# Performance work log

Measured on AMD Instinct MI355X. Metric: run time of the kernel, lower is better.

The kernel has to match this reference:

```python
import jax, jax.numpy as jnp
import numpy as np

N_NODES, N_EDGES, N_GRAPHS = 20000, 320000, 64
D_IN, D_H, D_FC, OUT_DIMS = 1280, 512, 1024, 5000
BN_EPS = 1e-5


def setup_inputs() -> dict:
    key = jax.random.key(0)
    ks = jax.random.split(key, 12)
    sc = lambda k, s: (jax.random.normal(k, s, jnp.float32) * 0.02)
    return {
        "x": jax.random.normal(ks[0], (N_NODES, D_IN), jnp.float32),
        "edge_index": jax.random.randint(ks[1], (2, N_EDGES), 0, N_NODES, dtype=jnp.int64),
        "batch": jnp.sort(jax.random.randint(ks[2], (N_NODES,), 0, N_GRAPHS, dtype=jnp.int64)),
        "Wg1": sc(ks[3], (D_IN, D_H)),
        "bg1": jnp.zeros((D_H,), jnp.float32),
        "Wg2": sc(ks[4], (D_H, D_H)),
        "bg2": jnp.zeros((D_H,), jnp.float32),
        "W1": sc(ks[5], (D_H, D_FC)),
        "b1": jnp.zeros((D_FC,), jnp.float32),
        "W2": sc(ks[6], (D_FC, OUT_DIMS)),
        "b2": jnp.zeros((OUT_DIMS,), jnp.float32),
        "gamma": jnp.ones((OUT_DIMS,), jnp.float32),
        "beta": jnp.zeros((OUT_DIMS,), jnp.float32),
    }


def _gcn_conv(h_in, W, b, src, dst):
    # PyG GCNConv: linear transform, symmetric deg^{-1/2} normalization with self-loops.
    h = h_in @ W  # [N, D]
    ones = jnp.ones((src.shape[0],), h.dtype)
    deg = jax.ops.segment_sum(ones, dst, num_segments=N_NODES) + 1.0  # self-loop
    dinv = jax.lax.rsqrt(deg)  # [N]
    coef = dinv[src] * dinv[dst]  # [E]
    agg = jax.ops.segment_sum(h[src] * coef[:, None], dst, num_segments=N_NODES)
    agg = agg + h * (dinv * dinv)[:, None]  # self-loop contribution
    return agg + b


def reference(x, edge_index, batch, Wg1, bg1, Wg2, bg2, W1, b1, W2, b2, gamma, beta):
    src, dst = edge_index[0], edge_index[1]
    h = jax.nn.relu(_gcn_conv(x, Wg1, bg1, src, dst))
    h = jax.nn.relu(_gcn_conv(h, Wg2, bg2, src, dst))
    # global max pool over each graph in the batch
    g = jax.ops.segment_max(h, batch, num_segments=N_GRAPHS)  # [G, 512]
    # fc head (eval mode: dropout = identity, BatchNorm1d uses running stats mean=0, var=1)
    h1 = jax.nn.relu(g @ W1 + b1)
    logits = h1 @ W2 + b2
    bn = logits * (gamma / jnp.sqrt(1.0 + BN_EPS)) + beta
    return jax.nn.sigmoid(bn)
```

## Files before the change

kernel.cpp:

```cpp
#include <hip/hip_runtime.h>
#include <math.h>

#define N_NODES 20000
#define N_EDGES 320000
#define N_GRAPHS 64
#define D_IN 1280
#define D_H 512
#define D_FC 1024
#define OUT_DIMS 5000
#define BKT_CAP 64
#define PSPLIT 8

typedef unsigned short ushort_t;
typedef short bf16x8 __attribute__((ext_vector_type(8)));
typedef float f32x4 __attribute__((ext_vector_type(4)));

__device__ __forceinline__ ushort_t f2b(float x) {
    unsigned u = __float_as_uint(x);
    unsigned r = (u + 0x7FFFu + ((u >> 16) & 1u)) >> 16;
    return (ushort_t)r;
}

#define WAITVM(n) asm volatile("s_waitcnt vmcnt(" #n ")" ::: "memory")
#define WAITLG() asm volatile("s_waitcnt lgkmcnt(0)" ::: "memory")
#define SCHED0() __builtin_amdgcn_sched_barrier(0)

#define GLL16(gp, lp)                                                                  \
    __builtin_amdgcn_global_load_lds((const __attribute__((address_space(1))) void*)(gp), \
                                     (__attribute__((address_space(3))) void*)(lp), 16, 0, 0)

__global__ __launch_bounds__(64) void mfma_gemm_1w(const ushort_t* __restrict__ A,
                                                   const ushort_t* __restrict__ BT,
                                                   ushort_t* __restrict__ C,
                                                   int M, int N, int K) {
    __shared__ ushort_t lds[8192];
    const int lane = threadIdx.x;
    const int lo = lane & 15, quad = lane >> 4;

    const int bid = blockIdx.x;
    const int v = (bid & 7) * 313 + (bid >> 3);
    const int rowBase = (v >> 3) * 64;
    const int colBase = (v & 7) * 64;

    const int q = (lane & 3) ^ ((lane >> 3) & 3);
    const int rb = lane >> 2;
    const ushort_t* pa[4];
    const ushort_t* pb[4];
#pragma unroll
    for (int i = 0; i < 4; ++i) {
        int ar = rowBase + rb + 16 * i;
        if (ar >= M) ar = M - 1;
        pa[i] = A + (size_t)ar * K + q * 8;
        pb[i] = BT + (size_t)(colBase + rb + 16 * i) * K + q * 8;
    }

#define ISSUE_TILE(p)                                      \
    {                                                      \
        GLL16(pa[0], lds + (p) * 2048 + 0 * 512);          \
        GLL16(pa[1], lds + (p) * 2048 + 1 * 512);          \
        GLL16(pa[2], lds + (p) * 2048 + 2 * 512);          \
        GLL16(pa[3], lds + (p) * 2048 + 3 * 512);          \
        GLL16(pb[0], lds + 4096 + (p) * 2048 + 0 * 512);   \
        GLL16(pb[1], lds + 4096 + (p) * 2048 + 1 * 512);   \
        GLL16(pb[2], lds + 4096 + (p) * 2048 + 2 * 512);   \
        GLL16(pb[3], lds + 4096 + (p) * 2048 + 3 * 512);   \
        pa[0] += 32; pa[1] += 32; pa[2] += 32; pa[3] += 32; \
        pb[0] += 32; pb[1] += 32; pb[2] += 32; pb[3] += 32; \
    }

    const int qs = (quad ^ ((lo >> 1) & 3)) * 8;
    int offA[4], offB[4];
#pragma unroll
    for (int i = 0; i < 4; ++i) offA[i] = (i * 16 + lo) * 32 + qs;
#pragma unroll
    for (int j = 0; j < 4; ++j) offB[j] = (j * 16 + lo) * 32 + qs;

    f32x4 acc[4][4] = {};
    const int NK = K >> 5;

    ISSUE_TILE(0);
    ISSUE_TILE(1);

    for (int k = 0; k < NK; ++k) {
        if (k + 1 < NK) { WAITVM(8); } else { WAITVM(0); }
        const ushort_t* Ab = lds + (k & 1) * 2048;
        const ushort_t* Bb = lds + 4096 + (k & 1) * 2048;
        bf16x8 af[4], bfr[4];
#pragma unroll
        for (int i = 0; i < 4; ++i) af[i] = *(const bf16x8*)&Ab[offA[i]];
#pragma unroll
        for (int j = 0; j < 4; ++j) bfr[j] = *(const bf16x8*)&Bb[offB[j]];
        WAITLG();
        if (k + 2 < NK) { ISSUE_TILE(k & 1); }
        SCHED0();
#pragma unroll
        for (int i = 0; i < 4; ++i)
#pragma unroll
            for (int j = 0; j < 4; ++j)
                acc[i][j] = __builtin_amdgcn_mfma_f32_16x16x32_bf16(af[i], bfr[j], acc[i][j], 0, 0, 0);
    }
#undef ISSUE_TILE

#pragma unroll
    for (int i = 0; i < 4; ++i) {
        int row0 = rowBase + i * 16 + quad * 4;
#pragma unroll
        for (int j = 0; j < 4; ++j) {
            int col = colBase + j * 16 + lo;
            if (col >= N) continue;
#pragma unroll
            for (int r = 0; r < 4; ++r) {
                int row = row0 + r;
                if (row < M) C[(size_t)row * N + col] = f2b(acc[i][j][r]);
            }
        }
    }
}

#define PREP_ZB 5
#define PREP_T1 640
#define PREP_T2 256
#define PREP_XB 12500
#define PREP_NBLK (PREP_ZB + PREP_T1 + PREP_T2 + PREP_XB + 1)

__global__ __launch_bounds__(256) void prep_all(const float* __restrict__ W1src, ushort_t* __restrict__ w1t,
                                                const float* __restrict__ W2src, ushort_t* __restrict__ w2t,
                                                const float* __restrict__ x, ushort_t* __restrict__ xb,
                                                int* __restrict__ zbase,
                                                const int* __restrict__ batch, int* __restrict__ gstart) {
    __shared__ float tile[32][33];
    int b = blockIdx.x;
    const int t = threadIdx.x;

    if (b < PREP_ZB) {
        int i = b * 256 + t;
        if (i < 1250) {
            int4* p = (int4*)zbase + (size_t)i * 4;
            int4 z = {0, 0, 0, 0};
            p[0] = z; p[1] = z; p[2] = z; p[3] = z;
        }
        return;
    }
    b -= PREP_ZB;

    if (b < PREP_T1 + PREP_T2) {
        const float* W;
        ushort_t* WT;
        int K, N, tb;
        if (b < PREP_T1) { W = W1src; WT = w1t; K = D_IN; N = D_H; tb = b; }
        else             { W = W2src; WT = w2t; K = D_H;  N = D_H; tb = b - PREP_T1; }
        const int ntn = N >> 5;
        const int kt = tb / ntn, nt = tb - kt * ntn;
        const int tx = t & 31, ty = t >> 5;
#pragma unroll
        for (int it = 0; it < 4; ++it) {
            int k = kt * 32 + ty + it * 8;
            tile[ty + it * 8][tx] = W[(size_t)k * N + nt * 32 + tx];
        }
        __syncthreads();
#pragma unroll
        for (int it = 0; it < 4; ++it) {
            int n = nt * 32 + ty + it * 8;
            WT[(size_t)n * K + kt * 32 + tx] = f2b(tile[tx][ty + it * 8]);
        }
        return;
    }
    b -= PREP_T1 + PREP_T2;

    if (b < PREP_XB) {
        int i = b * 256 + t;
        const float4* p = (const float4*)(x + (size_t)i * 8);
        float4 v0 = p[0], v1 = p[1];
        ushort_t w[8] = {f2b(v0.x), f2b(v0.y), f2b(v0.z), f2b(v0.w),
                         f2b(v1.x), f2b(v1.y), f2b(v1.z), f2b(v1.w)};
        *(uint4*)(xb + (size_t)i * 8) = *(uint4*)w;
        return;
    }

    if (t <= N_GRAPHS) {
        int lo = 0, hi = N_NODES;
        while (lo < hi) {
            int mid = (lo + hi) >> 1;
            if (batch[mid] < t) lo = mid + 1; else hi = mid;
        }
        gstart[t] = lo;
    }
}

__global__ void fill_bucket(const int* __restrict__ src, const int* __restrict__ dst,
                            int* __restrict__ cursor, int* __restrict__ col) {
    int e = blockIdx.x * blockDim.x + threadIdx.x;
    if (e < N_EDGES) {
        int d = dst[e];
        int p = atomicAdd(cursor + d, 1);
        if (p < BKT_CAP) col[(d << 6) + p] = src[e];
    }
}

__global__ void compute_dinv(const int* __restrict__ deg, float* __restrict__ dinv) {
    int v = blockIdx.x * blockDim.x + threadIdx.x;
    if (v < N_NODES) dinv[v] = rsqrtf((float)deg[v] + 1.0f);
}

__global__ __launch_bounds__(256) void gemm_splitk(const float* __restrict__ A,
                                                   const float* __restrict__ B,
                                                   float* __restrict__ P,
                                                   int M, int N, int K, int KC) {
    __shared__ float As[16][64];
    __shared__ float Bs[16][64];
    const int t = threadIdx.x;
    const int tx = t & 15, ty = t >> 4;
    const int rowBase = blockIdx.y * 64;
    const int colBase = blockIdx.x * 64;
    const int kbeg = blockIdx.z * KC;
    const int kend = kbeg + KC;
    float acc[4][4] = {};
    for (int k0 = kbeg; k0 < kend; k0 += 16) {
#pragma unroll
        for (int i = 0; i < 4; ++i) {
            int idx = t + i * 256;
            int row = idx >> 4, kk = idx & 15;
            int gr = rowBase + row;
            As[kk][row] = (gr < M) ? A[(size_t)gr * K + k0 + kk] : 0.f;
        }
#pragma unroll
        for (int i = 0; i < 4; ++i) {
            int idx = t + i * 256;
            int kk = idx >> 6, col = idx & 63;
            int gc = colBase + col;
            Bs[kk][col] = (gc < N) ? B[(size_t)(k0 + kk) * N + gc] : 0.f;
        }
        __syncthreads();
#pragma unroll
        for (int kk = 0; kk < 16; ++kk) {
            float a[4], bb[4];
#pragma unroll
            for (int i = 0; i < 4; ++i) a[i] = As[kk][ty * 4 + i];
#pragma unroll
            for (int j = 0; j < 4; ++j) bb[j] = Bs[kk][tx * 4 + j];
#pragma unroll
            for (int i = 0; i < 4; ++i)
#pragma unroll
                for (int j = 0; j < 4; ++j) acc[i][j] = fmaf(a[i], bb[j], acc[i][j]);
        }
        __syncthreads();
    }
    float* Pz = P + (size_t)blockIdx.z * M * N;
#pragma unroll
    for (int i = 0; i < 4; ++i) {
        int gr = rowBase + ty * 4 + i;
        if (gr >= M) continue;
#pragma unroll
        for (int j = 0; j < 4; ++j) {
            int gc = colBase + tx * 4 + j;
            if (gc < N) Pz[(size_t)gr * N + gc] = acc[i][j];
        }
    }
}

__global__ void reduce_bias_relu(const float* __restrict__ P, const float* __restrict__ b,
                                 float* __restrict__ out, int total, int N, int S) {
    int i = blockIdx.x * blockDim.x + threadIdx.x;
    if (i >= total) return;
    float s = 0.f;
    for (int z = 0; z < S; ++z) s += P[(size_t)z * total + i];
    out[i] = fmaxf(s + b[i % N], 0.f);
}

__global__ void reduce_bn_sigmoid(const float* __restrict__ P, const float* __restrict__ b2,
                                  const float* __restrict__ gamma, const float* __restrict__ beta,
                                  float* __restrict__ out, int S) {
    int i = blockIdx.x * blockDim.x + threadIdx.x;
    if (i >= N_GRAPHS * OUT_DIMS) return;
    int c = i % OUT_DIMS;
    float s = 0.f;
    for (int z = 0; z < S; ++z) s += P[(size_t)z * N_GRAPHS * OUT_DIMS + i];
    const float sc = 0.9999950000374997f;
    float zz = (s + b2[c]) * (gamma[c] * sc) + beta[c];
    out[i] = 1.f / (1.f + expf(-zz));
}

__device__ __forceinline__ void bf8_fma(uint4 v, float c, float* acc) {
    unsigned a[4] = {v.x, v.y, v.z, v.w};
#pragma unroll
    for (int i = 0; i < 4; ++i) {
        float lo = __uint_as_float(a[i] << 16);
        float hi = __uint_as_float(a[i] & 0xFFFF0000u);
        acc[2 * i]     = fmaf(lo, c, acc[2 * i]);
        acc[2 * i + 1] = fmaf(hi, c, acc[2 * i + 1]);
    }
}

__device__ __forceinline__ void agg_node_bf16(const ushort_t* __restrict__ H,
                                              const int* __restrict__ deg,
                                              const int* __restrict__ col,
                                              const float* __restrict__ dinv,
                                              const float* __restrict__ bias,
                                              int v, int f, float* r) {
    const int beg = v << 6;
    int d = deg[v]; if (d > BKT_CAP) d = BKT_CAP;
    const int end = beg + d;
    const float dv = dinv[v];
    float acc[8] = {};
    int j = beg;
    for (; j + 7 < end; j += 8) {
        int s[8];
#pragma unroll
        for (int u = 0; u < 8; ++u) s[u] = col[j + u];
        float c[8];
#pragma unroll
        for (int u = 0; u < 8; ++u) c[u] = dinv[s[u]] * dv;
        uint4 h[8];
#pragma unroll
        for (int u = 0; u < 8; ++u) h[u] = *(const uint4*)(H + (size_t)s[u] * D_H + f);
#pragma unroll
        for (int u = 0; u < 8; ++u) bf8_fma(h[u], c[u], acc);
    }
    for (; j + 3 < end; j += 4) {
        int s0 = col[j], s1 = col[j + 1], s2 = col[j + 2], s3 = col[j + 3];
        float c0 = dinv[s0] * dv, c1 = dinv[s1] * dv;
        float c2 = dinv[s2] * dv, c3 = dinv[s3] * dv;
        uint4 h0 = *(const uint4*)(H + (size_t)s0 * D_H + f);
        uint4 h1 = *(const uint4*)(H + (size_t)s1 * D_H + f);
        uint4 h2 = *(const uint4*)(H + (size_t)s2 * D_H + f);
        uint4 h3 = *(const uint4*)(H + (size_t)s3 * D_H + f);
        bf8_fma(h0, c0, acc);
        bf8_fma(h1, c1, acc);
        bf8_fma(h2, c2, acc);
        bf8_fma(h3, c3, acc);
    }
    for (; j < end; ++j) {
        int s0 = col[j];
        float c0 = dinv[s0] * dv;
        uint4 h0 = *(const uint4*)(H + (size_t)s0 * D_H + f);
        bf8_fma(h0, c0, acc);
    }
    uint4 hv = *(const uint4*)(H + (size_t)v * D_H + f);
    bf8_fma(hv, dv * dv, acc);
    float4 b0 = *(const float4*)(bias + f);
    float4 b1 = *(const float4*)(bias + f + 4);
    r[0] = fmaxf(acc[0] + b0.x, 0.f);
    r[1] = fmaxf(acc[1] + b0.y, 0.f);
    r[2] = fmaxf(acc[2] + b0.z, 0.f);
    r[3] = fmaxf(acc[3] + b0.w, 0.f);
    r[4] = fmaxf(acc[4] + b1.x, 0.f);
    r[5] = fmaxf(acc[5] + b1.y, 0.f);
    r[6] = fmaxf(acc[6] + b1.z, 0.f);
    r[7] = fmaxf(acc[7] + b1.w, 0.f);
}

__global__ __launch_bounds__(256) void gather_agg_relu_bf16(const ushort_t* __restrict__ H,
                                                            const int* __restrict__ deg,
                                                            const int* __restrict__ col,
                                                            const float* __restrict__ dinv,
                                                            const float* __restrict__ bias,
                                                            ushort_t* __restrict__ out) {
    const int v = blockIdx.x * 4 + (threadIdx.x >> 6);
    const int f = (threadIdx.x & 63) * 8;
    float r[8];
    agg_node_bf16(H, deg, col, dinv, bias, v, f, r);
    ushort_t o[8];
#pragma unroll
    for (int i = 0; i < 8; ++i) o[i] = f2b(r[i]);
    *(uint4*)(out + (size_t)v * D_H + f) = *(uint4*)o;
}

__global__ __launch_bounds__(256) void pool_max_partial(const ushort_t* __restrict__ h2,
                                                        const int* __restrict__ gstart,
                                                        float* __restrict__ pbuf) {
    const int g = blockIdx.x;
    const int s = blockIdx.y;
    const int f = threadIdx.x * 2;
    const int beg = gstart[g], end = gstart[g + 1];
    const int len = end - beg;
    const int chunk = (len + PSPLIT - 1) / PSPLIT;
    int lo = beg + s * chunk;
    int hi = lo + chunk; if (hi > end) hi = end;
    float m0 = -INFINITY, m1 = -INFINITY;
    int v = lo;
    for (; v + 3 < hi; v += 4) {
        unsigned u0 = *(const unsigned*)(h2 + (size_t)(v + 0) * D_H + f);
        unsigned u1 = *(const unsigned*)(h2 + (size_t)(v + 1) * D_H + f);
        unsigned u2 = *(const unsigned*)(h2 + (size_t)(v + 2) * D_H + f);
        unsigned u3 = *(const unsigned*)(h2 + (size_t)(v + 3) * D_H + f);
        m0 = fmaxf(m0, fmaxf(fmaxf(__uint_as_float(u0 << 16), __uint_as_float(u1 << 16)),
                             fmaxf(__uint_as_float(u2 << 16), __uint_as_float(u3 << 16))));
        m1 = fmaxf(m1, fmaxf(fmaxf(__uint_as_float(u0 & 0xFFFF0000u), __uint_as_float(u1 & 0xFFFF0000u)),
                             fmaxf(__uint_as_float(u2 & 0xFFFF0000u), __uint_as_float(u3 & 0xFFFF0000u))));
    }
    for (; v < hi; ++v) {
        unsigned u = *(const unsigned*)(h2 + (size_t)v * D_H + f);
        m0 = fmaxf(m0, __uint_as_float(u << 16));
        m1 = fmaxf(m1, __uint_as_float(u & 0xFFFF0000u));
    }
    float* p = pbuf + ((size_t)s * N_GRAPHS + g) * D_H + f;
    p[0] = m0;
    p[1] = m1;
}

__global__ void pool_max_final(const float* __restrict__ pbuf, float* __restrict__ gbuf) {
    int i = blockIdx.x * blockDim.x + threadIdx.x;
    if (i >= N_GRAPHS * D_H) return;
    float m = -INFINITY;
#pragma unroll
    for (int s = 0; s < PSPLIT; ++s) m = fmaxf(m, pbuf[(size_t)s * N_GRAPHS * D_H + i]);
    gbuf[i] = m;
}

extern "C" void kernel_launch(void* const* d_in, const int* in_sizes, int n_in,
                              void* d_out, int out_size, void* d_ws, size_t ws_size,
                              hipStream_t stream) {
    const float* x     = (const float*)d_in[0];
    const int*   ei    = (const int*)d_in[1];
    const int*   batch = (const int*)d_in[2];
    const float* Wg1   = (const float*)d_in[3];
    const float* bg1   = (const float*)d_in[4];
    const float* Wg2   = (const float*)d_in[5];
    const float* bg2   = (const float*)d_in[6];
    const float* W1    = (const float*)d_in[7];
    const float* b1    = (const float*)d_in[8];
    const float* W2    = (const float*)d_in[9];
    const float* b2    = (const float*)d_in[10];
    const float* gamma = (const float*)d_in[11];
    const float* beta  = (const float*)d_in[12];
    const int* src = ei;
    const int* dst = ei + N_EDGES;
    float* out = (float*)d_out;

    const int S1 = 8;
    const int S2 = 8;

    ushort_t* hpre   = (ushort_t*)d_ws;
    ushort_t* h1b    = hpre + (size_t)N_NODES * D_H;
    ushort_t* w1t    = h1b + (size_t)N_NODES * D_H;
    ushort_t* w2t    = w1t + (size_t)D_H * D_IN;
    ushort_t* xb     = w2t + (size_t)D_H * D_H;
    float*    dinv   = (float*)(xb + (size_t)N_NODES * D_IN);
    float*    gbuf   = dinv + N_NODES;
    float*    pbuf   = gbuf + N_GRAPHS * D_H;
    float*    fc1o   = pbuf + (size_t)PSPLIT * N_GRAPHS * D_H;
    float*    part1  = fc1o + N_GRAPHS * D_FC;
    float*    part2  = part1 + (size_t)S1 * N_GRAPHS * D_FC;
    int*      cursor = (int*)(part2 + (size_t)S2 * N_GRAPHS * OUT_DIMS);
    int*      colbkt = cursor + N_NODES;
    int*      gstart = colbkt + (size_t)N_NODES * BKT_CAP;

    prep_all<<<PREP_NBLK, 256, 0, stream>>>(Wg1, w1t, Wg2, w2t, x, xb, cursor, batch, gstart);

    fill_bucket<<<(N_EDGES + 255) / 256, 256, 0, stream>>>(src, dst, cursor, colbkt);
    compute_dinv<<<(N_NODES + 255) / 256, 256, 0, stream>>>(cursor, dinv);

    const int gconv = 2504;

    mfma_gemm_1w<<<gconv, 64, 0, stream>>>(xb, w1t, hpre, N_NODES, D_H, D_IN);
    gather_agg_relu_bf16<<<N_NODES / 4, 256, 0, stream>>>(hpre, cursor, colbkt, dinv, bg1, h1b);

    mfma_gemm_1w<<<gconv, 64, 0, stream>>>(h1b, w2t, hpre, N_NODES, D_H, D_H);
    gather_agg_relu_bf16<<<N_NODES / 4, 256, 0, stream>>>(hpre, cursor, colbkt, dinv, bg2, h1b);
    pool_max_partial<<<dim3(N_GRAPHS, PSPLIT), 256, 0, stream>>>(h1b, gstart, pbuf);
    pool_max_final<<<(N_GRAPHS * D_H + 255) / 256, 256, 0, stream>>>(pbuf, gbuf);

    dim3 gfc1((D_FC + 63) / 64, 1, S1);
    gemm_splitk<<<gfc1, 256, 0, stream>>>(gbuf, W1, part1, N_GRAPHS, D_FC, D_H, D_H / S1);
    reduce_bias_relu<<<(N_GRAPHS * D_FC + 255) / 256, 256, 0, stream>>>(
        part1, b1, fc1o, N_GRAPHS * D_FC, D_FC, S1);

    dim3 gfc2((OUT_DIMS + 63) / 64, 1, S2);
    gemm_splitk<<<gfc2, 256, 0, stream>>>(fc1o, W2, part2, N_GRAPHS, OUT_DIMS, D_FC, D_FC / S2);
    reduce_bn_sigmoid<<<(N_GRAPHS * OUT_DIMS + 255) / 256, 256, 0, stream>>>(
        part2, b2, gamma, beta, out, S2);
}
```

Measured before the change: 444.1 us.

## Fuse fp32-to-bf16 conversion of x into first GEMM and load operands directly

Drops the separate pass that converts x to bf16 and writes an xb buffer. The first GCN GEMM now reads fp32 x directly and converts it in registers with v_cvt_pk_bf16_f32. Both GEMMs stop staging tiles through LDS with global_load_lds and instead load MFMA fragments straight from global memory into registers, double-buffered. This saves the 51 MB x round trip and the LDS staging, but fp32 A loads double the bytes each block reads for A, and the per-lane direct loads are less coalesced with no LDS reuse.

Result: slower. 546.7 us (+23.1%).

```diff
diff --git a/kernel.cpp b/kernel.cpp
--- a/kernel.cpp
+++ b/kernel.cpp
@@ -21,85 +21,69 @@
     return (ushort_t)r;
 }
 
-#define WAITVM(n) asm volatile("s_waitcnt vmcnt(" #n ")" ::: "memory")
-#define WAITLG() asm volatile("s_waitcnt lgkmcnt(0)" ::: "memory")
-#define SCHED0() __builtin_amdgcn_sched_barrier(0)
-
-#define GLL16(gp, lp)                                                                  \
-    __builtin_amdgcn_global_load_lds((const __attribute__((address_space(1))) void*)(gp), \
-                                     (__attribute__((address_space(3))) void*)(lp), 16, 0, 0)
-
-__global__ __launch_bounds__(64) void mfma_gemm_1w(const ushort_t* __restrict__ A,
-                                                   const ushort_t* __restrict__ BT,
-                                                   ushort_t* __restrict__ C,
-                                                   int M, int N, int K) {
-    __shared__ ushort_t lds[8192];
+__device__ __forceinline__ unsigned cvt_pk(float lo, float hi) {
+    unsigned r;
+    asm("v_cvt_pk_bf16_f32 %0, %1, %2" : "=v"(r) : "v"(lo), "v"(hi));
+    return r;
+}
+
+__global__ __launch_bounds__(64) void gemm_dir_bf16(const ushort_t* __restrict__ A,
+                                                    const ushort_t* __restrict__ BT,
+                                                    ushort_t* __restrict__ C,
+                                                    int M, int N, int K) {
     const int lane = threadIdx.x;
     const int lo = lane & 15, quad = lane >> 4;
-
     const int bid = blockIdx.x;
     const int v = (bid & 7) * 313 + (bid >> 3);
     const int rowBase = (v >> 3) * 64;
     const int colBase = (v & 7) * 64;
 
-    const int q = (lane & 3) ^ ((lane >> 3) & 3);
-    const int rb = lane >> 2;
     const ushort_t* pa[4];
     const ushort_t* pb[4];
 #pragma unroll
     for (int i = 0; i < 4; ++i) {
-        int ar = rowBase + rb + 16 * i;
-        if (ar >= M) ar = M - 1;
-        pa[i] = A + (size_t)ar * K + q * 8;
-        pb[i] = BT + (size_t)(colBase + rb + 16 * i) * K + q * 8;
-    }
-
-#define ISSUE_TILE(p)                                      \
-    {                                                      \
-        GLL16(pa[0], lds + (p) * 2048 + 0 * 512);          \
-        GLL16(pa[1], lds + (p) * 2048 + 1 * 512);          \
-        GLL16(pa[2], lds + (p) * 2048 + 2 * 512);          \
-        GLL16(pa[3], lds + (p) * 2048 + 3 * 512);          \
-        GLL16(pb[0], lds + 4096 + (p) * 2048 + 0 * 512);   \
-        GLL16(pb[1], lds + 4096 + (p) * 2048 + 1 * 512);   \
-        GLL16(pb[2], lds + 4096 + (p) * 2048 + 2 * 512);   \
-        GLL16(pb[3], lds + 4096 + (p) * 2048 + 3 * 512);   \
-        pa[0] += 32; pa[1] += 32; pa[2] += 32; pa[3] += 32; \
-        pb[0] += 32; pb[1] += 32; pb[2] += 32; pb[3] += 32; \
-    }
-
-    const int qs = (quad ^ ((lo >> 1) & 3)) * 8;
-    int offA[4], offB[4];
-#pragma unroll
-    for (int i = 0; i < 4; ++i) offA[i] = (i * 16 + lo) * 32 + qs;
-#pragma unroll
-    for (int j = 0; j < 4; ++j) offB[j] = (j * 16 + lo) * 32 + qs;
+        int r = rowBase + i * 16 + lo;
+        if (r >= M) r = M - 1;
+        pa[i] = A + (size_t)r * K + quad * 8;
+        pb[i] = BT + (size_t)(colBase + i * 16 + lo) * K + quad * 8;
+    }
 
     f32x4 acc[4][4] = {};
     const int NK = K >> 5;
 
-    ISSUE_TILE(0);
-    ISSUE_TILE(1);
-
-    for (int k = 0; k < NK; ++k) {
-        if (k + 1 < NK) { WAITVM(8); } else { WAITVM(0); }
-        const ushort_t* Ab = lds + (k & 1) * 2048;
-        const ushort_t* Bb = lds + 4096 + (k & 1) * 2048;
-        bf16x8 af[4], bfr[4];
-#pragma unroll
-        for (int i = 0; i < 4; ++i) af[i] = *(const bf16x8*)&Ab[offA[i]];
-#pragma unroll
-        for (int j = 0; j < 4; ++j) bfr[j] = *(const bf16x8*)&Bb[offB[j]];
-        WAITLG();
-        if (k + 2 < NK) { ISSUE_TILE(k & 1); }
-        SCHED0();
+    bf16x8 a0[4], b0[4], a1[4], b1[4];
+#pragma unroll
+    for (int i = 0; i < 4; ++i) {
+        a0[i] = *(const bf16x8*)(pa[i]);
+        b0[i] = *(const bf16x8*)(pb[i]);
+    }
+
+    for (int kk = 0; kk < NK; kk += 2) {
+#pragma unroll
+        for (int i = 0; i < 4; ++i) {
+            a1[i] = *(const bf16x8*)(pa[i] + 32);
+            b1[i] = *(const bf16x8*)(pb[i] + 32);
+        }
 #pragma unroll
         for (int i = 0; i < 4; ++i)
 #pragma unroll
             for (int j = 0; j < 4; ++j)
-                acc[i][j] = __builtin_amdgcn_mfma_f32_16x16x32_bf16(af[i], bfr[j], acc[i][j], 0, 0, 0);
-    }
-#undef ISSUE_TILE
+                acc[i][j] = __builtin_amdgcn_mfma_f32_16x16x32_bf16(a0[i], b0[j], acc[i][j], 0, 0, 0);
+#pragma unroll
+        for (int i = 0; i < 4; ++i) { pa[i] += 64; pb[i] += 64; }
+        if (kk + 2 < NK) {
+#pragma unroll
+            for (int i = 0; i < 4; ++i) {
+                a0[i] = *(const bf16x8*)(pa[i]);
+                b0[i] = *(const bf16x8*)(pb[i]);
+            }
+        }
+#pragma unroll
+        for (int i = 0; i < 4; ++i)
+#pragma unroll
+            for (int j = 0; j < 4; ++j)
+                acc[i][j] = __builtin_amdgcn_mfma_f32_16x16x32_bf16(a1[i], b1[j], acc[i][j], 0, 0, 0);
+    }
 
 #pragma unroll
     for (int i = 0; i < 4; ++i) {
@@ -117,15 +101,94 @@
     }
 }
 
+__global__ __launch_bounds__(64) void gemm_dir_af32(const float* __restrict__ A,
+                                                    const ushort_t* __restrict__ BT,
+                                                    ushort_t* __restrict__ C,
+                                                    int M, int N, int K) {
+    const int lane = threadIdx.x;
+    const int lo = lane & 15, quad = lane >> 4;
+    const int bid = blockIdx.x;
+    const int v = (bid & 7) * 313 + (bid >> 3);
+    const int rowBase = (v >> 3) * 64;
+    const int colBase = (v & 7) * 64;
+
+    const float* pa[4];
+    const ushort_t* pb[4];
+#pragma unroll
+    for (int i = 0; i < 4; ++i) {
+        int r = rowBase + i * 16 + lo;
+        if (r >= M) r = M - 1;
+        pa[i] = A + (size_t)r * K + quad * 8;
+        pb[i] = BT + (size_t)(colBase + i * 16 + lo) * K + quad * 8;
+    }
+
+#define LDA(dst, off)                                                     \
+    {                                                                     \
+        _Pragma("unroll") for (int i = 0; i < 4; ++i) {                   \
+            float4 f0 = *(const float4*)(pa[i] + (off));                  \
+            float4 f1 = *(const float4*)(pa[i] + (off) + 4);              \
+            uint4 u;                                                     \
+            u.x = cvt_pk(f0.x, f0.y); u.y = cvt_pk(f0.z, f0.w);          \
+            u.z = cvt_pk(f1.x, f1.y); u.w = cvt_pk(f1.z, f1.w);          \
+            dst[i] = *(bf16x8*)&u;                                       \
+        }                                                                 \
+    }
+
+    f32x4 acc[4][4] = {};
+    const int NK = K >> 5;
+
+    bf16x8 a0[4], b0[4], a1[4], b1[4];
+    LDA(a0, 0);
+#pragma unroll
+    for (int i = 0; i < 4; ++i) b0[i] = *(const bf16x8*)(pb[i]);
+
+    for (int kk = 0; kk < NK; kk += 2) {
+        LDA(a1, 32);
+#pragma unroll
+        for (int i = 0; i < 4; ++i) b1[i] = *(const bf16x8*)(pb[i] + 32);
+#pragma unroll
+        for (int i = 0; i < 4; ++i)
+#pragma unroll
+            for (int j = 0; j < 4; ++j)
+                acc[i][j] = __builtin_amdgcn_mfma_f32_16x16x32_bf16(a0[i], b0[j], acc[i][j], 0, 0, 0);
+#pragma unroll
+        for (int i = 0; i < 4; ++i) { pa[i] += 64; pb[i] += 64; }
+        if (kk + 2 < NK) {
+            LDA(a0, 0);
+#pragma unroll
+            for (int i = 0; i < 4; ++i) b0[i] = *(const bf16x8*)(pb[i]);
+        }
+#pragma unroll
+        for (int i = 0; i < 4; ++i)
+#pragma unroll
+            for (int j = 0; j < 4; ++j)
+                acc[i][j] = __builtin_amdgcn_mfma_f32_16x16x32_bf16(a1[i], b1[j], acc[i][j], 0, 0, 0);
+    }
+#undef LDA
+
+#pragma unroll
+    for (int i = 0; i < 4; ++i) {
+        int row0 = rowBase + i * 16 + quad * 4;
+#pragma unroll
+        for (int j = 0; j < 4; ++j) {
+            int col = colBase + j * 16 + lo;
+            if (col >= N) continue;
+#pragma unroll
+            for (int r = 0; r < 4; ++r) {
+                int row = row0 + r;
+                if (row < M) C[(size_t)row * N + col] = f2b(acc[i][j][r]);
+            }
+        }
+    }
+}
+
 #define PREP_ZB 5
 #define PREP_T1 640
 #define PREP_T2 256
-#define PREP_XB 12500
-#define PREP_NBLK (PREP_ZB + PREP_T1 + PREP_T2 + PREP_XB + 1)
+#define PREP_NBLK (PREP_ZB + PREP_T1 + PREP_T2 + 1)
 
 __global__ __launch_bounds__(256) void prep_all(const float* __restrict__ W1src, ushort_t* __restrict__ w1t,
                                                 const float* __restrict__ W2src, ushort_t* __restrict__ w2t,
-                                                const float* __restrict__ x, ushort_t* __restrict__ xb,
                                                 int* __restrict__ zbase,
                                                 const int* __restrict__ batch, int* __restrict__ gstart) {
     __shared__ float tile[32][33];
@@ -163,17 +226,6 @@
             int n = nt * 32 + ty + it * 8;
             WT[(size_t)n * K + kt * 32 + tx] = f2b(tile[tx][ty + it * 8]);
         }
-        return;
-    }
-    b -= PREP_T1 + PREP_T2;
-
-    if (b < PREP_XB) {
-        int i = b * 256 + t;
-        const float4* p = (const float4*)(x + (size_t)i * 8);
-        float4 v0 = p[0], v1 = p[1];
-        ushort_t w[8] = {f2b(v0.x), f2b(v0.y), f2b(v0.z), f2b(v0.w),
-                         f2b(v1.x), f2b(v1.y), f2b(v1.z), f2b(v1.w)};
-        *(uint4*)(xb + (size_t)i * 8) = *(uint4*)w;
         return;
     }
 
@@ -434,8 +486,7 @@
     ushort_t* h1b    = hpre + (size_t)N_NODES * D_H;
     ushort_t* w1t    = h1b + (size_t)N_NODES * D_H;
     ushort_t* w2t    = w1t + (size_t)D_H * D_IN;
-    ushort_t* xb     = w2t + (size_t)D_H * D_H;
-    float*    dinv   = (float*)(xb + (size_t)N_NODES * D_IN);
+    float*    dinv   = (float*)(w2t + (size_t)D_H * D_H);
     float*    gbuf   = dinv + N_NODES;
     float*    pbuf   = gbuf + N_GRAPHS * D_H;
     float*    fc1o   = pbuf + (size_t)PSPLIT * N_GRAPHS * D_H;
@@ -445,17 +496,17 @@
     int*      colbkt = cursor + N_NODES;
     int*      gstart = colbkt + (size_t)N_NODES * BKT_CAP;
 
-    prep_all<<<PREP_NBLK, 256, 0, stream>>>(Wg1, w1t, Wg2, w2t, x, xb, cursor, batch, gstart);
+    prep_all<<<PREP_NBLK, 256, 0, stream>>>(Wg1, w1t, Wg2, w2t, cursor, batch, gstart);
 
     fill_bucket<<<(N_EDGES + 255) / 256, 256, 0, stream>>>(src, dst, cursor, colbkt);
     compute_dinv<<<(N_NODES + 255) / 256, 256, 0, stream>>>(cursor, dinv);
 
     const int gconv = 2504;
 
-    mfma_gemm_1w<<<gconv, 64, 0, stream>>>(xb, w1t, hpre, N_NODES, D_H, D_IN);
+    gemm_dir_af32<<<gconv, 64, 0, stream>>>(x, w1t, hpre, N_NODES, D_H, D_IN);
     gather_agg_relu_bf16<<<N_NODES / 4, 256, 0, stream>>>(hpre, cursor, colbkt, dinv, bg1, h1b);
 
-    mfma_gemm_1w<<<gconv, 64, 0, stream>>>(h1b, w2t, hpre, N_NODES, D_H, D_H);
+    gemm_dir_bf16<<<gconv, 64, 0, stream>>>(h1b, w2t, hpre, N_NODES, D_H, D_H);
     gather_agg_relu_bf16<<<N_NODES / 4, 256, 0, stream>>>(hpre, cursor, colbkt, dinv, bg2, h1b);
     pool_max_partial<<<dim3(N_GRAPHS, PSPLIT), 256, 0, stream>>>(h1b, gstart, pbuf);
     pool_max_final<<<(N_GRAPHS * D_H + 255) / 256, 256, 0, stream>>>(pbuf, gbuf);
```

## Fuse fp32-to-bf16 conversion of x into first GCN GEMM and triple-buffer LDS

Applied to the files above, without the earlier changes.

Drops the separate pass that converted x to bf16 in the prep kernel. A new GEMM variant reads fp32 rows of x directly into registers, packs them with v_cvt_pk_bf16_f32 and writes them into swizzled LDS, while B still streams in via global_load_lds. Both GEMMs move to a three-stage LDS ring, so the lgkmcnt wait and scheduling barrier before issuing the next tile can go. The aim is to remove the write and re-read of a large bf16 copy of x. In exchange each A tile is fetched as fp32 (twice the bytes per GEMM load, repeated across column blocks) and the GEMMs use more LDS and registers.

After: 497.3 us. 12.0% more time.

```diff
diff --git a/kernel.cpp b/kernel.cpp
--- a/kernel.cpp
+++ b/kernel.cpp
@@ -21,22 +21,26 @@
     return (ushort_t)r;
 }
 
+__device__ __forceinline__ unsigned cvt_pk(float lo, float hi) {
+    unsigned r;
+    asm("v_cvt_pk_bf16_f32 %0, %1, %2" : "=v"(r) : "v"(lo), "v"(hi));
+    return r;
+}
+
 #define WAITVM(n) asm volatile("s_waitcnt vmcnt(" #n ")" ::: "memory")
 #define WAITLG() asm volatile("s_waitcnt lgkmcnt(0)" ::: "memory")
-#define SCHED0() __builtin_amdgcn_sched_barrier(0)
 
 #define GLL16(gp, lp)                                                                  \
     __builtin_amdgcn_global_load_lds((const __attribute__((address_space(1))) void*)(gp), \
                                      (__attribute__((address_space(3))) void*)(lp), 16, 0, 0)
 
-__global__ __launch_bounds__(64) void mfma_gemm_1w(const ushort_t* __restrict__ A,
+__global__ __launch_bounds__(64) void gemm_1w_bf16(const ushort_t* __restrict__ A,
                                                    const ushort_t* __restrict__ BT,
                                                    ushort_t* __restrict__ C,
                                                    int M, int N, int K) {
-    __shared__ ushort_t lds[8192];
+    __shared__ ushort_t lds[12288];
     const int lane = threadIdx.x;
     const int lo = lane & 15, quad = lane >> 4;
-
     const int bid = blockIdx.x;
     const int v = (bid & 7) * 313 + (bid >> 3);
     const int rowBase = (v >> 3) * 64;
@@ -54,16 +58,16 @@
         pb[i] = BT + (size_t)(colBase + rb + 16 * i) * K + q * 8;
     }
 
-#define ISSUE_TILE(p)                                      \
+#define ISSUE_TILE(POFF)                                   \
     {                                                      \
-        GLL16(pa[0], lds + (p) * 2048 + 0 * 512);          \
-        GLL16(pa[1], lds + (p) * 2048 + 1 * 512);          \
-        GLL16(pa[2], lds + (p) * 2048 + 2 * 512);          \
-        GLL16(pa[3], lds + (p) * 2048 + 3 * 512);          \
-        GLL16(pb[0], lds + 4096 + (p) * 2048 + 0 * 512);   \
-        GLL16(pb[1], lds + 4096 + (p) * 2048 + 1 * 512);   \
-        GLL16(pb[2], lds + 4096 + (p) * 2048 + 2 * 512);   \
-        GLL16(pb[3], lds + 4096 + (p) * 2048 + 3 * 512);   \
+        GLL16(pa[0], lds + (POFF) + 0 * 512);              \
+        GLL16(pa[1], lds + (POFF) + 1 * 512);              \
+        GLL16(pa[2], lds + (POFF) + 2 * 512);              \
+        GLL16(pa[3], lds + (POFF) + 3 * 512);              \
+        GLL16(pb[0], lds + 6144 + (POFF) + 0 * 512);       \
+        GLL16(pb[1], lds + 6144 + (POFF) + 1 * 512);       \
+        GLL16(pb[2], lds + 6144 + (POFF) + 2 * 512);       \
+        GLL16(pb[3], lds + 6144 + (POFF) + 3 * 512);       \
         pa[0] += 32; pa[1] += 32; pa[2] += 32; pa[3] += 32; \
         pb[0] += 32; pb[1] += 32; pb[2] += 32; pb[3] += 32; \
     }
@@ -79,25 +83,28 @@
     const int NK = K >> 5;
 
     ISSUE_TILE(0);
-    ISSUE_TILE(1);
-
+    ISSUE_TILE(2048);
+
+    int cur = 0;
     for (int k = 0; k < NK; ++k) {
         if (k + 1 < NK) { WAITVM(8); } else { WAITVM(0); }
-        const ushort_t* Ab = lds + (k & 1) * 2048;
-        const ushort_t* Bb = lds + 4096 + (k & 1) * 2048;
+        const ushort_t* Ab = lds + cur;
+        const ushort_t* Bb = lds + 6144 + cur;
         bf16x8 af[4], bfr[4];
 #pragma unroll
         for (int i = 0; i < 4; ++i) af[i] = *(const bf16x8*)&Ab[offA[i]];
 #pragma unroll
         for (int j = 0; j < 4; ++j) bfr[j] = *(const bf16x8*)&Bb[offB[j]];
-        WAITLG();
-        if (k + 2 < NK) { ISSUE_TILE(k & 1); }
-        SCHED0();
+        if (k + 2 < NK) {
+            int nn = cur + 4096; if (nn >= 6144) nn -= 6144;
+            ISSUE_TILE(nn);
+        }
 #pragma unroll
         for (int i = 0; i < 4; ++i)
 #pragma unroll
             for (int j = 0; j < 4; ++j)
                 acc[i][j] = __builtin_amdgcn_mfma_f32_16x16x32_bf16(af[i], bfr[j], acc[i][j], 0, 0, 0);
+        cur += 2048; if (cur >= 6144) cur = 0;
     }
 #undef ISSUE_TILE
 
@@ -117,15 +124,144 @@
     }
 }
 
+__global__ __launch_bounds__(64) void gemm_1w_af32(const float* __restrict__ A,
+                                                   const ushort_t* __restrict__ BT,
+                                                   ushort_t* __restrict__ C,
+                                                   int M, int N, int K) {
+    __shared__ ushort_t lds[12288];
+    const int lane = threadIdx.x;
+    const int lo = lane & 15, quad = lane >> 4;
+    const int bid = blockIdx.x;
+    const int v = (bid & 7) * 313 + (bid >> 3);
+    const int rowBase = (v >> 3) * 64;
+    const int colBase = (v & 7) * 64;
+
+    const int q = (lane & 3) ^ ((lane >> 3) & 3);
+    const int rb = lane >> 2;
+    const ushort_t* pb[4];
+#pragma unroll
+    for (int i = 0; i < 4; ++i)
+        pb[i] = BT + (size_t)(colBase + rb + 16 * i) * K + q * 8;
+
+#define ISSUE_B(POFF)                                      \
+    {                                                      \
+        GLL16(pb[0], lds + 6144 + (POFF) + 0 * 512);       \
+        GLL16(pb[1], lds + 6144 + (POFF) + 1 * 512);       \
+        GLL16(pb[2], lds + 6144 + (POFF) + 2 * 512);       \
+        GLL16(pb[3], lds + 6144 + (POFF) + 3 * 512);       \
+        pb[0] += 32; pb[1] += 32; pb[2] += 32; pb[3] += 32; \
+    }
+
+    int ar = rowBase + lane; if (ar >= M) ar = M - 1;
+    const float* pA = A + (size_t)ar * K;
+    const int swA = (lane >> 1) & 3;
+    int wrA[4];
+#pragma unroll
+    for (int j = 0; j < 4; ++j) wrA[j] = lane * 32 + ((j ^ swA) * 8);
+
+    float4 vA0_0, vA0_1, vA0_2, vA0_3, vA0_4, vA0_5, vA0_6, vA0_7;
+    float4 vA1_0, vA1_1, vA1_2, vA1_3, vA1_4, vA1_5, vA1_6, vA1_7;
+
+#define LOADA(S)                                   \
+    {                                              \
+        vA##S##_0 = *(const float4*)(pA + 0);      \
+        vA##S##_1 = *(const float4*)(pA + 4);      \
+        vA##S##_2 = *(const float4*)(pA + 8);      \
+        vA##S##_3 = *(const float4*)(pA + 12);     \
+        vA##S##_4 = *(const float4*)(pA + 16);     \
+        vA##S##_5 = *(const float4*)(pA + 20);     \
+        vA##S##_6 = *(const float4*)(pA + 24);     \
+        vA##S##_7 = *(const float4*)(pA + 28);     \
+        pA += 32;                                  \
+    }
+#define WRITEA(S, POFF)                                                           \
+    {                                                                             \
+        uint4 u;                                                                  \
+        u.x = cvt_pk(vA##S##_0.x, vA##S##_0.y); u.y = cvt_pk(vA##S##_0.z, vA##S##_0.w); \
+        u.z = cvt_pk(vA##S##_1.x, vA##S##_1.y); u.w = cvt_pk(vA##S##_1.z, vA##S##_1.w); \
+        *(uint4*)&lds[(POFF) + wrA[0]] = u;                                       \
+        u.x = cvt_pk(vA##S##_2.x, vA##S##_2.y); u.y = cvt_pk(vA##S##_2.z, vA##S##_2.w); \
+        u.z = cvt_pk(vA##S##_3.x, vA##S##_3.y); u.w = cvt_pk(vA##S##_3.z, vA##S##_3.w); \
+        *(uint4*)&lds[(POFF) + wrA[1]] = u;                                       \
+        u.x = cvt_pk(vA##S##_4.x, vA##S##_4.y); u.y = cvt_pk(vA##S##_4.z, vA##S##_4.w); \
+        u.z = cvt_pk(vA##S##_5.x, vA##S##_5.y); u.w = cvt_pk(vA##S##_5.z, vA##S##_5.w); \
+        *(uint4*)&lds[(POFF) + wrA[2]] = u;                                       \
+        u.x = cvt_pk(vA##S##_6.x, vA##S##_6.y); u.y = cvt_pk(vA##S##_6.z, vA##S##_6.w); \
+        u.z = cvt_pk(vA##S##_7.x, vA##S##_7.y); u.w = cvt_pk(vA##S##_7.z, vA##S##_7.w); \
+        *(uint4*)&lds[(POFF) + wrA[3]] = u;                                       \
+    }
+
+    const int qs = (quad ^ ((lo >> 1) & 3)) * 8;
+    int offA[4], offB[4];
+#pragma unroll
+    for (int i = 0; i < 4; ++i) offA[i] = (i * 16 + lo) * 32 + qs;
+#pragma unroll
+    for (int j = 0; j < 4; ++j) offB[j] = (j * 16 + lo) * 32 + qs;
+
+    f32x4 acc[4][4] = {};
+    const int NK = K >> 5;
+
+    ISSUE_B(0);
+    LOADA(0);
+    ISSUE_B(2048);
+    WRITEA(0, 0);
+    LOADA(1);
+
+#define AF32_BODY(kv, SL, SW)                                                          \
+    {                                                                                  \
+        const int k_ = (kv);                                                           \
+        WAITLG();            \
+        const ushort_t* Ab = lds + cur;                                                \
+        const ushort_t* Bb = lds + 6144 + cur;                                         \
+        bf16x8 af[4], bfr[4];                                                          \
+        _Pragma("unroll") for (int i = 0; i < 4; ++i) af[i] = *(const bf16x8*)&Ab[offA[i]]; \
+        _Pragma("unroll") for (int j = 0; j < 4; ++j) bfr[j] = *(const bf16x8*)&Bb[offB[j]]; \
+        int nxt = cur + 2048; if (nxt >= 6144) nxt = 0;                                \
+        if (k_ + 2 < NK) {                                                             \
+            int nn = cur + 4096; if (nn >= 6144) nn -= 6144;                           \
+            ISSUE_B(nn);                                                 \
+            LOADA(SL);                                                   \
+        }                                                                              \
+        if (k_ + 1 < NK) { WRITEA(SW, nxt); }    \
+        _Pragma("unroll") for (int i = 0; i < 4; ++i)                                  \
+            _Pragma("unroll") for (int j = 0; j < 4; ++j)                              \
+                acc[i][j] = __builtin_amdgcn_mfma_f32_16x16x32_bf16(af[i], bfr[j], acc[i][j], 0, 0, 0); \
+        cur = nxt;                                                                     \
+    }
+
+    int cur = 0;
+    for (int kk = 0; kk < NK; kk += 2) {
+        AF32_BODY(kk, 0, 1);
+        AF32_BODY(kk + 1, 1, 0);
+    }
+#undef AF32_BODY
+#undef ISSUE_B
+#undef LOADA
+#undef WRITEA
+
+#pragma unroll
+    for (int i = 0; i < 4; ++i) {
+        int row0 = rowBase + i * 16 + quad * 4;
+#pragma unroll
+        for (int j = 0; j < 4; ++j) {
+            int col = colBase + j * 16 + lo;
+            if (col >= N) continue;
+#pragma unroll
+            for (int r = 0; r < 4; ++r) {
+                int row = row0 + r;
+                if (row < M) C[(size_t)row * N + col] = f2b(acc[i][j][r]);
+            }
+        }
+    }
+}
+
 #define PREP_ZB 5
 #define PREP_T1 640
 #define PREP_T2 256
-#define PREP_XB 12500
-#define PREP_NBLK (PREP_ZB + PREP_T1 + PREP_T2 + PREP_XB + 1)
+#define PREP_NBLK (PREP_ZB + PREP_T1 + PREP_T2 + 1)
 
 __global__ __launch_bounds__(256) void prep_all(const float* __restrict__ W1src, ushort_t* __restrict__ w1t,
                                                 const float* __restrict__ W2src, ushort_t* __restrict__ w2t,
-                                                const float* __restrict__ x, ushort_t* __restrict__ xb,
                                                 int* __restrict__ zbase,
                                                 const int* __restrict__ batch, int* __restrict__ gstart) {
     __shared__ float tile[32][33];
@@ -163,17 +299,6 @@
             int n = nt * 32 + ty + it * 8;
             WT[(size_t)n * K + kt * 32 + tx] = f2b(tile[tx][ty + it * 8]);
         }
-        return;
-    }
-    b -= PREP_T1 + PREP_T2;
-
-    if (b < PREP_XB) {
-        int i = b * 256 + t;
-        const float4* p = (const float4*)(x + (size_t)i * 8);
-        float4 v0 = p[0], v1 = p[1];
-        ushort_t w[8] = {f2b(v0.x), f2b(v0.y), f2b(v0.z), f2b(v0.w),
-                         f2b(v1.x), f2b(v1.y), f2b(v1.z), f2b(v1.w)};
-        *(uint4*)(xb + (size_t)i * 8) = *(uint4*)w;
         return;
     }
 
@@ -434,8 +559,7 @@
     ushort_t* h1b    = hpre + (size_t)N_NODES * D_H;
     ushort_t* w1t    = h1b + (size_t)N_NODES * D_H;
     ushort_t* w2t    = w1t + (size_t)D_H * D_IN;
-    ushort_t* xb     = w2t + (size_t)D_H * D_H;
-    float*    dinv   = (float*)(xb + (size_t)N_NODES * D_IN);
+    float*    dinv   = (float*)(w2t + (size_t)D_H * D_H);
     float*    gbuf   = dinv + N_NODES;
     float*    pbuf   = gbuf + N_GRAPHS * D_H;
     float*    fc1o   = pbuf + (size_t)PSPLIT * N_GRAPHS * D_H;
@@ -445,17 +569,17 @@
     int*      colbkt = cursor + N_NODES;
     int*      gstart = colbkt + (size_t)N_NODES * BKT_CAP;
 
-    prep_all<<<PREP_NBLK, 256, 0, stream>>>(Wg1, w1t, Wg2, w2t, x, xb, cursor, batch, gstart);
+    prep_all<<<PREP_NBLK, 256, 0, stream>>>(Wg1, w1t, Wg2, w2t, cursor, batch, gstart);
 
     fill_bucket<<<(N_EDGES + 255) / 256, 256, 0, stream>>>(src, dst, cursor, colbkt);
     compute_dinv<<<(N_NODES + 255) / 256, 256, 0, stream>>>(cursor, dinv);
 
     const int gconv = 2504;
 
-    mfma_gemm_1w<<<gconv, 64, 0, stream>>>(xb, w1t, hpre, N_NODES, D_H, D_IN);
+    gemm_1w_af32<<<gconv, 64, 0, stream>>>(x, w1t, hpre, N_NODES, D_H, D_IN);
     gather_agg_relu_bf16<<<N_NODES / 4, 256, 0, stream>>>(hpre, cursor, colbkt, dinv, bg1, h1b);
 
-    mfma_gemm_1w<<<gconv, 64, 0, stream>>>(h1b, w2t, hpre, N_NODES, D_H, D_H);
+    gemm_1w_bf16<<<gconv, 64, 0, stream>>>(h1b, w2t, hpre, N_NODES, D_H, D_H);
     gather_agg_relu_bf16<<<N_NODES / 4, 256, 0, stream>>>(hpre, cursor, colbkt, dinv, bg2, h1b);
     pool_max_partial<<<dim3(N_GRAPHS, PSPLIT), 256, 0, stream>>>(h1b, gstart, pbuf);
     pool_max_final<<<(N_GRAPHS * D_H + 255) / 256, 256, 0, stream>>>(pbuf, gbuf);
```
